# Kernel tuning notes

Hardware: AMD Instinct MI355X
Metric: run time of the kernel (lower is better)

Reference implementation:

```python
import jax, jax.numpy as jnp
import numpy as np

COST_CLASS, COST_MASK, COST_DICE = 2.0, 5.0, 5.0
NUM_POINTS = 12544

def setup_inputs() -> dict:
    key = jax.random.key(0)
    k1, k2, k3, k4, k5 = jax.random.split(key, 5)
    bs, Q, K = 4, 100, 134
    H = W = 256
    M = 80
    P = H * W
    pred_logits = jax.random.normal(k1, (bs, Q, K), dtype=jnp.float32)
    pred_masks = jax.random.normal(k2, (bs, Q, H, W), dtype=jnp.float32)
    tgt_labels = jax.random.randint(k3, (M,), 0, K - 1, dtype=jnp.int32)
    # binary target masks, stored as float (matches .float() in torch code)
    tgt_masks = (jax.random.uniform(k4, (M, H, W)) > 0.5).astype(jnp.float32)
    # random subset of points without replacement (torch.randperm[:num_points])
    point_idx = jax.random.permutation(k5, P)[:NUM_POINTS].astype(jnp.int32)
    return {"pred_logits": pred_logits, "pred_masks": pred_masks,
            "tgt_labels": tgt_labels, "tgt_masks": tgt_masks,
            "point_idx": point_idx}

def reference(pred_logits, pred_masks, tgt_labels, tgt_masks, point_idx):
    bs, Q, K = pred_logits.shape
    N = bs * Q
    M = tgt_masks.shape[0]
    Pn = point_idx.shape[0]

    # class cost: -p[n, tgt_id[m]]
    out_prob = jax.nn.softmax(pred_logits.reshape(N, K), axis=-1)
    tgt_ids = jnp.clip(tgt_labels.astype(jnp.int32), 0, K - 1)
    cost_class = -out_prob[:, tgt_ids]                      # (N, M)

    # sampled mask logits / targets
    x = pred_masks.reshape(N, -1)[:, point_idx]             # (N, Pn) logits
    y = tgt_masks.reshape(M, -1)[:, point_idx]              # (M, Pn) binary float

    # BCE-with-logits cost, separable form:
    # mean_p[softplus(x) - x*y] = mean_p softplus(x) - (x @ y^T)/Pn
    sp_mean = jnp.mean(jax.nn.softplus(x), axis=-1)         # (N,)
    xy = jnp.einsum('np,mp->nm', x, y)                      # (N, M)
    cost_mask = sp_mean[:, None] - xy / Pn

    # dice cost
    s = jax.nn.sigmoid(x)                                   # (N, Pn)
    numer = 2.0 * jnp.einsum('np,mp->nm', s, y)             # (N, M)
    denom = jnp.sum(s, axis=-1)[:, None] + jnp.sum(y, axis=-1)[None, :]
    cost_dice = 1.0 - (numer + 1.0) / (denom + 1.0)

    C = COST_CLASS * cost_class + COST_MASK * cost_mask + COST_DICE * cost_dice
    return C.reshape(bs, Q, M)
```

## Files before the change

### kernel.cpp

```cpp
#include <hip/hip_runtime.h>
#include <math.h>

#define N_ROWS 400
#define M_ROWS 80
#define K_CLS  134
#define PN     12544
#define PFULL  65536
#define NSUB   25
#define TSTEPS 392
#define KSPLIT 196
#define TPB    2
#define KCG    49

#define GY_BLOCKS 245

typedef __attribute__((ext_vector_type(4))) float  f32x4;
typedef __attribute__((ext_vector_type(8))) __bf16 bf16x8;

__device__ __forceinline__ float wave_reduce_sum(float v) {
#pragma unroll
    for (int off = 32; off > 0; off >>= 1) v += __shfl_down(v, off, 64);
    return v;
}

__global__ __launch_bounds__(1024) void sort_softmax_kernel(
        const int* __restrict__ point_idx, int* __restrict__ sel,
        const float* __restrict__ pred_logits,
        float* __restrict__ rowmax, float* __restrict__ rowsum) {
    int tid = threadIdx.x;
    if (blockIdx.x == 0) {
        __shared__ unsigned int bits[PFULL / 32];
        __shared__ int wtot[16], wbase[16];
        bits[tid] = 0u; bits[tid + 1024] = 0u;
        __syncthreads();
        for (int i = tid; i < PN; i += 1024) {
            int p = point_idx[i];
            atomicOr(&bits[p >> 5], 1u << (p & 31));
        }
        __syncthreads();
        unsigned int w0 = bits[tid * 2], w1 = bits[tid * 2 + 1];
        int cnt = __popc(w0) + __popc(w1);
        int lane = tid & 63, wid = tid >> 6;
        int v = cnt;
#pragma unroll
        for (int off = 1; off < 64; off <<= 1) {
            int u = __shfl_up(v, off, 64);
            if (lane >= off) v += u;
        }
        if (lane == 63) wtot[wid] = v;
        __syncthreads();
        if (tid == 0) {
            int run = 0;
#pragma unroll
            for (int i = 0; i < 16; ++i) { wbase[i] = run; run += wtot[i]; }
        }
        __syncthreads();
        int base = wbase[wid] + (v - cnt);
        int p0 = tid * 64;
        while (w0) { int b = __builtin_ctz(w0); w0 &= w0 - 1; sel[base++] = p0 + b; }
        p0 += 32;
        while (w1) { int b = __builtin_ctz(w1); w1 &= w1 - 1; sel[base++] = p0 + b; }
    } else {
        int wave = tid >> 6, lane = tid & 63;
        int n = (blockIdx.x - 1) * 16 + wave;
        const float* row = pred_logits + n * K_CLS;
        float mx = -1e30f;
        for (int k = lane; k < K_CLS; k += 64) mx = fmaxf(mx, row[k]);
#pragma unroll
        for (int off = 32; off > 0; off >>= 1) mx = fmaxf(mx, __shfl_down(mx, off, 64));
        mx = __shfl(mx, 0, 64);
        float se = 0.f;
        for (int k = lane; k < K_CLS; k += 64) se += expf(row[k] - mx);
        se = wave_reduce_sum(se);
        if (lane == 0) { rowmax[n] = mx; rowsum[n] = se; }
    }
}

__global__ __launch_bounds__(512) void gather_y_kernel(
        const float* __restrict__ tgt_masks, const int* __restrict__ sel,
        __bf16* __restrict__ Yb, float* __restrict__ ypart) {
    __shared__ float smem[128];
    int b = blockIdx.x;
    int j = b / 49, tch = b % 49;
    int wave = threadIdx.x >> 6, lane = threadIdx.x & 63;
    int colL = lane & 15, quad = lane >> 4;
    int m = 16 * j + colL;
    int t = tch * 8 + wave;
    int k0 = t * 32 + quad * 8;
    const float* yrow = tgt_masks + (size_t)m * PFULL;
    int idx[8];
    *(int4*)(idx)     = *(const int4*)(sel + k0);
    *(int4*)(idx + 4) = *(const int4*)(sel + k0 + 4);
    bf16x8 v; float acc = 0.f;
#pragma unroll
    for (int jj = 0; jj < 8; ++jj) {
        float y = yrow[idx[jj]];
        v[jj] = (__bf16)y;
        acc += y;
    }
    ((bf16x8*)Yb)[(size_t)(t * 5 + j) * 64 + lane] = v;
    acc += __shfl_down(acc, 32, 64);
    acc += __shfl_down(acc, 16, 64);
    if (quad == 0) smem[wave * 16 + colL] = acc;
    __syncthreads();
    if (threadIdx.x < 16) {
        float s = 0.f;
#pragma unroll
        for (int wv = 0; wv < 8; ++wv) s += smem[wv * 16 + threadIdx.x];
        ypart[tch * M_ROWS + 16 * j + threadIdx.x] = s;
    }
}

__global__ __launch_bounds__(256) void gemm_fused_kernel(
        const float* __restrict__ pred_masks, const int* __restrict__ sel,
        const __bf16* __restrict__ Yb,
        float* __restrict__ xypart, float* __restrict__ sypart,
        float* __restrict__ rowS, float* __restrict__ rowSP) {
    __shared__ float red[4][40][64];
    __shared__ float rowred[4][2][16];
    int wave = threadIdx.x >> 6, lane = threadIdx.x & 63;
    int nsub = blockIdx.x / KCG, kcg = blockIdx.x % KCG;
    int kc = kcg * 4 + wave;
    int n0 = nsub * 16;
    int colL = lane & 15, quad = lane >> 4;
    int tbase = kc * TPB;

    const float* row = pred_masks + (size_t)(n0 + colL) * PFULL;
    const bf16x8* Yfrag = (const bf16x8*)Yb;

    f32x4 accX[5], accS[5];
    f32x4 zero = {0.f, 0.f, 0.f, 0.f};
#pragma unroll
    for (int j = 0; j < 5; ++j) { accX[j] = zero; accS[j] = zero; }
    float sumS = 0.f, sumSP = 0.f;

    float xs[TPB][8];
    bf16x8 Bbuf[TPB][5];
#pragma unroll
    for (int i = 0; i < TPB; ++i) {
        int t = tbase + i;
        int k0 = t * 32 + quad * 8;
        int idx[8];
        *(int4*)(idx)     = *(const int4*)(sel + k0);
        *(int4*)(idx + 4) = *(const int4*)(sel + k0 + 4);
#pragma unroll
        for (int jj = 0; jj < 8; ++jj) xs[i][jj] = row[idx[jj]];
        const bf16x8* q = Yfrag + (size_t)(t * 5) * 64 + lane;
#pragma unroll
        for (int j = 0; j < 5; ++j) Bbuf[i][j] = q[(size_t)j * 64];
    }
#pragma unroll
    for (int i = 0; i < TPB; ++i) {
        bf16x8 aX, aS;
#pragma unroll
        for (int jj = 0; jj < 8; ++jj) {
            float x  = xs[i][jj];
            float ax = fabsf(x);
            float e  = __expf(-ax);
            float inv = __builtin_amdgcn_rcpf(1.f + e);
            float sig = (x >= 0.f) ? inv : e * inv;
            float sp  = fmaxf(x, 0.f) + __logf(1.f + e);
            aX[jj] = (__bf16)x; aS[jj] = (__bf16)sig;
            sumS += sig; sumSP += sp;
        }
#pragma unroll
        for (int j = 0; j < 5; ++j) {
            accX[j] = __builtin_amdgcn_mfma_f32_16x16x32_bf16(aX, Bbuf[i][j], accX[j], 0, 0, 0);
            accS[j] = __builtin_amdgcn_mfma_f32_16x16x32_bf16(aS, Bbuf[i][j], accS[j], 0, 0, 0);
        }
    }

#pragma unroll
    for (int j = 0; j < 5; ++j)
#pragma unroll
        for (int r = 0; r < 4; ++r) {
            red[wave][j * 4 + r][lane]      = accX[j][r];
            red[wave][20 + j * 4 + r][lane] = accS[j][r];
        }
    sumS  += __shfl_down(sumS, 32, 64);
    sumS  += __shfl_down(sumS, 16, 64);
    sumSP += __shfl_down(sumSP, 32, 64);
    sumSP += __shfl_down(sumSP, 16, 64);
    if (lane < 16) { rowred[wave][0][lane] = sumS; rowred[wave][1][lane] = sumSP; }
    __syncthreads();
#pragma unroll
    for (int v0 = 0; v0 < 10; ++v0) {
        int v = wave * 10 + v0;
        float s = red[0][v][lane] + red[1][v][lane] + red[2][v][lane] + red[3][v][lane];
        int vv = (v < 20) ? v : v - 20;
        int j = vv >> 2, r = vv & 3;
        int n = n0 + quad * 4 + r, m = 16 * j + colL;
        float* dst = (v < 20) ? xypart : sypart;
        dst[(size_t)kcg * (N_ROWS * M_ROWS) + n * M_ROWS + m] = s;
    }
    if (threadIdx.x < 16) {
        rowS[kcg * N_ROWS + n0 + threadIdx.x] =
            rowred[0][0][threadIdx.x] + rowred[1][0][threadIdx.x] +
            rowred[2][0][threadIdx.x] + rowred[3][0][threadIdx.x];
    } else if (threadIdx.x < 32) {
        int l = threadIdx.x - 16;
        rowSP[kcg * N_ROWS + n0 + l] =
            rowred[0][1][l] + rowred[1][1][l] + rowred[2][1][l] + rowred[3][1][l];
    }
}

__global__ void combine_kernel(const float* __restrict__ logits,
                               const int* __restrict__ tgt_labels,
                               const float* __restrict__ rowmax,
                               const float* __restrict__ rowsum,
                               const float* __restrict__ rowS,
                               const float* __restrict__ rowSP,
                               const float* __restrict__ ypart,
                               const float* __restrict__ xypart,
                               const float* __restrict__ sypart,
                               float* __restrict__ out) {
    int idx = blockIdx.x * blockDim.x + threadIdx.x;
    if (idx >= N_ROWS * M_ROWS) return;
    int n = idx / M_ROWS, m = idx % M_ROWS;
    float xy = 0.f, sy = 0.f, ssumv = 0.f, spsumv = 0.f, ysum = 0.f;
#pragma unroll 7
    for (int g = 0; g < KCG; ++g) {
        xy += xypart[(size_t)g * (N_ROWS * M_ROWS) + idx];
        sy += sypart[(size_t)g * (N_ROWS * M_ROWS) + idx];
        ssumv  += rowS[g * N_ROWS + n];
        spsumv += rowSP[g * N_ROWS + n];
        ysum += ypart[g * M_ROWS + m];
    }
    int tid = tgt_labels[m];
    tid = min(max(tid, 0), K_CLS - 1);
    float p = expf(logits[n * K_CLS + tid] - rowmax[n]) / rowsum[n];
    float cost_class = -p;
    float cost_mask = (spsumv - xy) * (1.0f / PN);
    float cost_dice = 1.f - (2.f * sy + 1.f) / (ssumv + ysum + 1.f);
    out[idx] = 2.f * cost_class + 5.f * cost_mask + 5.f * cost_dice;
}

extern "C" void kernel_launch(void* const* d_in, const int* in_sizes, int n_in,
                              void* d_out, int out_size, void* d_ws, size_t ws_size,
                              hipStream_t stream) {
    const float* pred_logits = (const float*)d_in[0];
    const float* pred_masks  = (const float*)d_in[1];
    const int*   tgt_labels  = (const int*)d_in[2];
    const float* tgt_masks   = (const float*)d_in[3];
    const int*   point_idx   = (const int*)d_in[4];
    float* out = (float*)d_out;

    char* ws = (char*)d_ws;
    size_t off = 0;
    auto carve = [&](size_t nbytes) {
        char* p = ws + off;
        off += (nbytes + 255) & ~(size_t)255;
        return p;
    };
    int*   sel    = (int*)carve(PN * 4);
    float* rowmax = (float*)carve(N_ROWS * 4);
    float* rowsum = (float*)carve(N_ROWS * 4);
    float* ypart  = (float*)carve(KCG * M_ROWS * 4);
    float* rowS   = (float*)carve(KCG * N_ROWS * 4);
    float* rowSP  = (float*)carve(KCG * N_ROWS * 4);
    float* xypart = (float*)carve((size_t)KCG * N_ROWS * M_ROWS * 4);
    float* sypart = (float*)carve((size_t)KCG * N_ROWS * M_ROWS * 4);
    __bf16* Yb = (__bf16*)carve((size_t)TSTEPS * 5 * 1024);
    (void)ws_size; (void)in_sizes; (void)n_in; (void)out_size;

    sort_softmax_kernel<<<26, 1024, 0, stream>>>(point_idx, sel, pred_logits, rowmax, rowsum);
    gather_y_kernel<<<GY_BLOCKS, 512, 0, stream>>>(tgt_masks, sel, Yb, ypart);
    gemm_fused_kernel<<<NSUB * KCG, 256, 0, stream>>>(
        pred_masks, sel, Yb, xypart, sypart, rowS, rowSP);
    combine_kernel<<<(N_ROWS * M_ROWS + 255) / 256, 256, 0, stream>>>(
        pred_logits, tgt_labels, rowmax, rowsum, rowS, rowSP, ypart, xypart, sypart, out);
}
```

Measured before the change: 217.1 us.

## Stream-compact pred_masks into dense bf16 rows before GEMM instead of gathering

```diff
diff --git a/kernel.cpp b/kernel.cpp
--- a/kernel.cpp
+++ b/kernel.cpp
@@ -8,10 +8,10 @@
 #define PFULL  65536
 #define NSUB   25
 #define TSTEPS 392
-#define KSPLIT 196
 #define TPB    2
 #define KCG    49
 
+#define CX_BLOCKS 3200
 #define GY_BLOCKS 245
 
 typedef __attribute__((ext_vector_type(4))) float  f32x4;
@@ -25,6 +25,7 @@
 
 __global__ __launch_bounds__(1024) void sort_softmax_kernel(
         const int* __restrict__ point_idx, int* __restrict__ sel,
+        unsigned int* __restrict__ bitsG, int* __restrict__ kbase,
         const float* __restrict__ pred_logits,
         float* __restrict__ rowmax, float* __restrict__ rowsum) {
     int tid = threadIdx.x;
@@ -38,6 +39,7 @@
             atomicOr(&bits[p >> 5], 1u << (p & 31));
         }
         __syncthreads();
+        bitsG[tid] = bits[tid]; bitsG[tid + 1024] = bits[tid + 1024];
         unsigned int w0 = bits[tid * 2], w1 = bits[tid * 2 + 1];
         int cnt = __popc(w0) + __popc(w1);
         int lane = tid & 63, wid = tid >> 6;
@@ -56,6 +58,7 @@
         }
         __syncthreads();
         int base = wbase[wid] + (v - cnt);
+        if ((tid & 15) == 0) kbase[tid >> 4] = base;
         int p0 = tid * 64;
         while (w0) { int b = __builtin_ctz(w0); w0 &= w0 - 1; sel[base++] = p0 + b; }
         p0 += 32;
@@ -76,44 +79,79 @@
     }
 }
 
-__global__ __launch_bounds__(512) void gather_y_kernel(
-        const float* __restrict__ tgt_masks, const int* __restrict__ sel,
-        __bf16* __restrict__ Yb, float* __restrict__ ypart) {
-    __shared__ float smem[128];
+__global__ __launch_bounds__(256) void stage2_kernel(
+        const float* __restrict__ pred_masks, const float* __restrict__ tgt_masks,
+        const int* __restrict__ sel, const unsigned int* __restrict__ bitsG,
+        const int* __restrict__ kbase,
+        __bf16* __restrict__ Xb, __bf16* __restrict__ Yb, float* __restrict__ ypart) {
+    __shared__ float smem[64];
     int b = blockIdx.x;
-    int j = b / 49, tch = b % 49;
     int wave = threadIdx.x >> 6, lane = threadIdx.x & 63;
-    int colL = lane & 15, quad = lane >> 4;
-    int m = 16 * j + colL;
-    int t = tch * 8 + wave;
-    int k0 = t * 32 + quad * 8;
-    const float* yrow = tgt_masks + (size_t)m * PFULL;
-    int idx[8];
-    *(int4*)(idx)     = *(const int4*)(sel + k0);
-    *(int4*)(idx + 4) = *(const int4*)(sel + k0 + 4);
-    bf16x8 v; float acc = 0.f;
-#pragma unroll
-    for (int jj = 0; jj < 8; ++jj) {
-        float y = yrow[idx[jj]];
-        v[jj] = (__bf16)y;
-        acc += y;
-    }
-    ((bf16x8*)Yb)[(size_t)(t * 5 + j) * 64 + lane] = v;
-    acc += __shfl_down(acc, 32, 64);
-    acc += __shfl_down(acc, 16, 64);
-    if (quad == 0) smem[wave * 16 + colL] = acc;
-    __syncthreads();
-    if (threadIdx.x < 16) {
-        float s = 0.f;
-#pragma unroll
-        for (int wv = 0; wv < 8; ++wv) s += smem[wv * 16 + threadIdx.x];
-        ypart[tch * M_ROWS + 16 * j + threadIdx.x] = s;
-    }
-}
-
-__global__ __launch_bounds__(256) void gemm_fused_kernel(
-        const float* __restrict__ pred_masks, const int* __restrict__ sel,
-        const __bf16* __restrict__ Yb,
+    if (b < CX_BLOCKS) {
+        int r = b >> 3, i8 = b & 7;
+        const float* row = pred_masks + (size_t)r * PFULL;
+        __bf16* xr = Xb + (size_t)r * PN;
+        int e = i8 * 8192 + wave * 2048;
+        int base = kbase[e >> 10];
+        unsigned long long below = (1ULL << lane) - 1;
+#pragma unroll
+        for (int win = 0; win < 8; ++win) {
+            int e0 = e + win * 256;
+            float xv[4]; unsigned int wrd[4];
+#pragma unroll
+            for (int j = 0; j < 4; ++j) {
+                int ei = e0 + j * 64 + lane;
+                xv[j]  = row[ei];
+                wrd[j] = bitsG[ei >> 5];
+            }
+#pragma unroll
+            for (int j = 0; j < 4; ++j) {
+                int bit = (wrd[j] >> (lane & 31)) & 1;
+                unsigned long long bal = __ballot(bit);
+                if (bit) {
+                    int rank = __popcll(bal & below);
+                    xr[base + rank] = (__bf16)xv[j];
+                }
+                base += __popcll(bal);
+            }
+        }
+    } else {
+        int bb = b - CX_BLOCKS;
+        int j = bb / 49, tch = bb % 49;
+        int colL = lane & 15, quad = lane >> 4;
+        int m = 16 * j + colL;
+        const float* yrow = tgt_masks + (size_t)m * PFULL;
+        float acc = 0.f;
+#pragma unroll
+        for (int u = 0; u < 2; ++u) {
+            int t = tch * 8 + wave * 2 + u;
+            int k0 = t * 32 + quad * 8;
+            int idx[8];
+            *(int4*)(idx)     = *(const int4*)(sel + k0);
+            *(int4*)(idx + 4) = *(const int4*)(sel + k0 + 4);
+            bf16x8 v;
+#pragma unroll
+            for (int jj = 0; jj < 8; ++jj) {
+                float y = yrow[idx[jj]];
+                v[jj] = (__bf16)y;
+                acc += y;
+            }
+            ((bf16x8*)Yb)[(size_t)(t * 5 + j) * 64 + lane] = v;
+        }
+        acc += __shfl_down(acc, 32, 64);
+        acc += __shfl_down(acc, 16, 64);
+        if (quad == 0) smem[wave * 16 + colL] = acc;
+        __syncthreads();
+        if (threadIdx.x < 16) {
+            float s = smem[threadIdx.x] + smem[16 + threadIdx.x] +
+                      smem[32 + threadIdx.x] + smem[48 + threadIdx.x];
+            ypart[tch * M_ROWS + 16 * j + threadIdx.x] = s;
+        }
+    }
+}
+
+__global__ __launch_bounds__(256) void gemm_kernel(
+        const __bf16* __restrict__ Xb, const __bf16* __restrict__ Yb,
         float* __restrict__ xypart, float* __restrict__ sypart,
         float* __restrict__ rowS, float* __restrict__ rowSP) {
     __shared__ float red[4][40][64];
@@ -125,7 +163,7 @@
     int colL = lane & 15, quad = lane >> 4;
     int tbase = kc * TPB;
 
-    const float* row = pred_masks + (size_t)(n0 + colL) * PFULL;
+    const __bf16* xrow = Xb + (size_t)(n0 + colL) * PN;
     const bf16x8* Yfrag = (const bf16x8*)Yb;
 
     f32x4 accX[5], accS[5];
@@ -134,39 +172,33 @@
     for (int j = 0; j < 5; ++j) { accX[j] = zero; accS[j] = zero; }
     float sumS = 0.f, sumSP = 0.f;
 
-    float xs[TPB][8];
-    bf16x8 Bbuf[TPB][5];
+    bf16x8 Av[TPB], Bbuf[TPB][5];
 #pragma unroll
     for (int i = 0; i < TPB; ++i) {
         int t = tbase + i;
-        int k0 = t * 32 + quad * 8;
-        int idx[8];
-        *(int4*)(idx)     = *(const int4*)(sel + k0);
-        *(int4*)(idx + 4) = *(const int4*)(sel + k0 + 4);
-#pragma unroll
-        for (int jj = 0; jj < 8; ++jj) xs[i][jj] = row[idx[jj]];
+        Av[i] = *(const bf16x8*)(xrow + (size_t)t * 32 + quad * 8);
         const bf16x8* q = Yfrag + (size_t)(t * 5) * 64 + lane;
 #pragma unroll
         for (int j = 0; j < 5; ++j) Bbuf[i][j] = q[(size_t)j * 64];
     }
 #pragma unroll
     for (int i = 0; i < TPB; ++i) {
-        bf16x8 aX, aS;
+        bf16x8 aS;
 #pragma unroll
         for (int jj = 0; jj < 8; ++jj) {
-            float x  = xs[i][jj];
+            float x  = (float)Av[i][jj];
             float ax = fabsf(x);
             float e  = __expf(-ax);
             float inv = __builtin_amdgcn_rcpf(1.f + e);
             float sig = (x >= 0.f) ? inv : e * inv;
             float sp  = fmaxf(x, 0.f) + __logf(1.f + e);
-            aX[jj] = (__bf16)x; aS[jj] = (__bf16)sig;
+            aS[jj] = (__bf16)sig;
             sumS += sig; sumSP += sp;
         }
 #pragma unroll
         for (int j = 0; j < 5; ++j) {
-            accX[j] = __builtin_amdgcn_mfma_f32_16x16x32_bf16(aX, Bbuf[i][j], accX[j], 0, 0, 0);
-            accS[j] = __builtin_amdgcn_mfma_f32_16x16x32_bf16(aS, Bbuf[i][j], accS[j], 0, 0, 0);
+            accX[j] = __builtin_amdgcn_mfma_f32_16x16x32_bf16(Av[i], Bbuf[i][j], accX[j], 0, 0, 0);
+            accS[j] = __builtin_amdgcn_mfma_f32_16x16x32_bf16(aS,    Bbuf[i][j], accS[j], 0, 0, 0);
         }
     }
 
@@ -252,21 +284,26 @@
         off += (nbytes + 255) & ~(size_t)255;
         return p;
     };
-    int*   sel    = (int*)carve(PN * 4);
-    float* rowmax = (float*)carve(N_ROWS * 4);
-    float* rowsum = (float*)carve(N_ROWS * 4);
-    float* ypart  = (float*)carve(KCG * M_ROWS * 4);
-    float* rowS   = (float*)carve(KCG * N_ROWS * 4);
-    float* rowSP  = (float*)carve(KCG * N_ROWS * 4);
-    float* xypart = (float*)carve((size_t)KCG * N_ROWS * M_ROWS * 4);
-    float* sypart = (float*)carve((size_t)KCG * N_ROWS * M_ROWS * 4);
-    __bf16* Yb = (__bf16*)carve((size_t)TSTEPS * 5 * 1024);
+    int*      sel    = (int*)carve(PN * 4);
+    unsigned* bitsG  = (unsigned*)carve((PFULL / 32) * 4);
+    int*      kbase  = (int*)carve(64 * 4);
+    float*    rowmax = (float*)carve(N_ROWS * 4);
+    float*    rowsum = (float*)carve(N_ROWS * 4);
+    float*    ypart  = (float*)carve(KCG * M_ROWS * 4);
+    float*    rowS   = (float*)carve(KCG * N_ROWS * 4);
+    float*    rowSP  = (float*)carve(KCG * N_ROWS * 4);
+    float*    xypart = (float*)carve((size_t)KCG * N_ROWS * M_ROWS * 4);
+    float*    sypart = (float*)carve((size_t)KCG * N_ROWS * M_ROWS * 4);
+    __bf16*   Xb     = (__bf16*)carve((size_t)N_ROWS * PN * 2);
+    __bf16*   Yb     = (__bf16*)carve((size_t)TSTEPS * 5 * 1024);
     (void)ws_size; (void)in_sizes; (void)n_in; (void)out_size;
 
-    sort_softmax_kernel<<<26, 1024, 0, stream>>>(point_idx, sel, pred_logits, rowmax, rowsum);
-    gather_y_kernel<<<GY_BLOCKS, 512, 0, stream>>>(tgt_masks, sel, Yb, ypart);
-    gemm_fused_kernel<<<NSUB * KCG, 256, 0, stream>>>(
-        pred_masks, sel, Yb, xypart, sypart, rowS, rowSP);
+    sort_softmax_kernel<<<26, 1024, 0, stream>>>(
+        point_idx, sel, bitsG, kbase, pred_logits, rowmax, rowsum);
+    stage2_kernel<<<CX_BLOCKS + GY_BLOCKS, 256, 0, stream>>>(
+        pred_masks, tgt_masks, sel, bitsG, kbase, Xb, Yb, ypart);
+    gemm_kernel<<<NSUB * KCG, 256, 0, stream>>>(
+        Xb, Yb, xypart, sypart, rowS, rowSP);
     combine_kernel<<<(N_ROWS * M_ROWS + 255) / 256, 256, 0, stream>>>(
         pred_logits, tgt_labels, rowmax, rowsum, rowS, rowSP, ypart, xypart, sypart, out);
 }
```

After: 232.8 us. +7.2%, slower.
